# Kernel tuning notes

Hardware: AMD Instinct MI355X
Metric: run time of the kernel (lower is better)

The kernel has to match this reference:

```python
import jax, jax.numpy as jnp
import numpy as np

D = 1024      # in/out token dims
E = 2048      # expanded dim = 2*D
S_ATT = 128   # attention feature dim s
EPS = 1e-5
SQRT_S = np.sqrt(S_ATT).astype(np.float32)


def setup_inputs() -> dict:
    key = jax.random.key(0)
    ks = jax.random.split(key, 8)
    B, S = 4, 2048
    x = jax.random.normal(ks[0], (B, S, D), dtype=jnp.float32)
    pos_enc = jax.random.normal(ks[1], (S, S_ATT), dtype=jnp.float32)
    # uv Linear: xavier_uniform on weight of shape [2e+s, D]
    fan_out = 2 * E + S_ATT
    limit = np.sqrt(6.0 / (D + fan_out)).astype(np.float32)
    uv_w = jax.random.uniform(ks[2], (fan_out, D), dtype=jnp.float32, minval=-limit, maxval=limit)
    # o Linear: default kaiming-uniform-ish; plain uniform works for a reference
    lim_o = np.sqrt(1.0 / E).astype(np.float32)
    o_w = jax.random.uniform(ks[3], (D, E), dtype=jnp.float32, minval=-lim_o, maxval=lim_o)
    gamma = jax.random.uniform(ks[4], (2, S_ATT), dtype=jnp.float32)
    beta = jax.random.uniform(ks[5], (2, S_ATT), dtype=jnp.float32)
    ln_g = jnp.ones((), dtype=jnp.float32)          # ScaleNorm learnable scalar
    res_scale = jnp.ones((D,), dtype=jnp.float32)   # ChannelWiseScale
    return {"x": x, "pos_enc": pos_enc, "uv_w": uv_w, "o_w": o_w,
            "gamma": gamma, "beta": beta, "ln_g": ln_g, "res_scale": res_scale}


def _gau(x, pos_enc, uv_w, o_w, gamma, beta, ln_g, res_scale):
    # ScaleNorm: x / max(||x|| * d^-0.5, eps) * g
    norm = jnp.linalg.norm(x, axis=-1, keepdims=True) * (D ** -0.5)
    xn = x / jnp.maximum(norm, EPS) * ln_g
    uv = jax.nn.silu(jnp.einsum('bsd,fd->bsf', xn, uv_w))  # [B,S,2E+s]
    u, v, base = uv[..., :E], uv[..., E:2 * E], uv[..., 2 * E:]
    # per-head affine: base[...,None,:]*gamma+beta -> q,k
    qk_base = base[..., None, :] * gamma + beta             # [B,S,2,s]
    q = qk_base[..., 0, :] + pos_enc[None, :, :]            # 'add' pos enc
    k = qk_base[..., 1, :] + pos_enc[None, :, :]
    scores = jnp.einsum('bqs,bks->bqk', q, k) / SQRT_S
    kernel = jnp.square(jax.nn.relu(scores))                # squared-ReLU attention
    attn_v = jnp.einsum('bqk,bke->bqe', kernel, v)
    out = jnp.einsum('bqe,de->bqd', u * attn_v, o_w)
    # residual shortcut with channel-wise scale (in == out dims)
    return x * res_scale + out


def reference(x, pos_enc, uv_w, o_w, gamma, beta, ln_g, res_scale):
    return _gau(x, pos_enc, uv_w, o_w, gamma, beta, ln_g, res_scale)
```

## Files before the change

kernel.cpp:

```cpp
#include <hip/hip_runtime.h>

typedef unsigned short u16;
typedef __bf16 bf16x8 __attribute__((ext_vector_type(8)));
typedef float f32x4 __attribute__((ext_vector_type(4)));

#define SEQ   2048
#define DDIM  1024
#define EDIM  2048
#define FDIM  4224
#define SATT  128
#define NBATCH 4

__device__ __forceinline__ u16 f2bf(float f) {
  unsigned u = __float_as_uint(f);
  unsigned r = (u + 0x7fffu + ((u >> 16) & 1u)) >> 16;
  return (u16)r;
}
__device__ __forceinline__ float bf2f(u16 v) {
  return __uint_as_float(((unsigned)v) << 16);
}

__device__ __forceinline__ void gload16(const u16* g, u16* l) {
  auto gp = (const __attribute__((address_space(1))) u16*)(unsigned long long)g;
  auto lp = (__attribute__((address_space(3))) u16*)(unsigned)(unsigned long long)l;
  __builtin_amdgcn_global_load_lds(gp, lp, 16, 0, 0);
}


__global__ void cvt_bf16_kernel(const float* __restrict__ in, u16* __restrict__ out, int n4) {
  int i = blockIdx.x * blockDim.x + threadIdx.x;
  if (i >= n4) return;
  float4 v = reinterpret_cast<const float4*>(in)[i];
  unsigned p0 = (unsigned)f2bf(v.x) | ((unsigned)f2bf(v.y) << 16);
  unsigned p1 = (unsigned)f2bf(v.z) | ((unsigned)f2bf(v.w) << 16);
  uint2 pk; pk.x = p0; pk.y = p1;
  reinterpret_cast<uint2*>(out)[i] = pk;
}

__global__ void rms_kernel(const float* __restrict__ x, const float* __restrict__ ln_g,
                           u16* __restrict__ xn) {
  int row = blockIdx.x;
  int t = threadIdx.x;
  const float4* xr = reinterpret_cast<const float4*>(x + (size_t)row * DDIM);
  float4 v = xr[t];
  float s = v.x * v.x + v.y * v.y + v.z * v.z + v.w * v.w;
#pragma unroll
  for (int off = 32; off > 0; off >>= 1) s += __shfl_down(s, off);
  __shared__ float wsum[4];
  int lane = t & 63, wv = t >> 6;
  if (lane == 0) wsum[wv] = s;
  __syncthreads();
  float tot = wsum[0] + wsum[1] + wsum[2] + wsum[3];
  float rms = sqrtf(tot * (1.0f / (float)DDIM));
  float scale = ln_g[0] / fmaxf(rms, 1e-5f);
  unsigned p0 = (unsigned)f2bf(v.x * scale) | ((unsigned)f2bf(v.y * scale) << 16);
  unsigned p1 = (unsigned)f2bf(v.z * scale) | ((unsigned)f2bf(v.w * scale) << 16);
  uint2 pk; pk.x = p0; pk.y = p1;
  reinterpret_cast<uint2*>(xn + (size_t)row * DDIM)[t] = pk;
}

__global__ void qk_kernel(const u16* __restrict__ uv, const float* __restrict__ pos_enc,
                          const float* __restrict__ gamma, const float* __restrict__ beta,
                          u16* __restrict__ q, u16* __restrict__ k, int ldF) {
  int r = blockIdx.x;
  int t = threadIdx.x;
  int s = r & (SEQ - 1);
  float bval = bf2f(uv[(size_t)r * ldF + 2 * EDIM + t]);
  float pe = pos_enc[(size_t)s * SATT + t];
  float qv = bval * gamma[t] + beta[t] + pe;
  float kv = bval * gamma[SATT + t] + beta[SATT + t] + pe;
  q[(size_t)r * SATT + t] = f2bf(qv);
  k[(size_t)r * SATT + t] = f2bf(kv);
}

__global__ void transpose_v(const u16* __restrict__ uv, u16* __restrict__ vt, int ldF) {
  __shared__ u16 tile[32][33];
  int b = blockIdx.z;
  uv += (size_t)b * SEQ * ldF;
  vt += (size_t)b * EDIM * SEQ;
  int e0 = blockIdx.x * 32, s0 = blockIdx.y * 32;
  int tx = threadIdx.x, ty = threadIdx.y;
#pragma unroll
  for (int j = 0; j < 32; j += 8)
    tile[ty + j][tx] = uv[(size_t)(s0 + ty + j) * ldF + EDIM + e0 + tx];
  __syncthreads();
#pragma unroll
  for (int j = 0; j < 32; j += 8)
    vt[(size_t)(e0 + ty + j) * SEQ + s0 + tx] = tile[tx][ty + j];
}

template <int EPI>
__global__ __launch_bounds__(512, 2) void gemm_bt3(
    const u16* __restrict__ A, const u16* __restrict__ B,
    int N, int K,
    u16* __restrict__ Cbf,
    const u16* __restrict__ U, int ldu,
    size_t sA, size_t sB, size_t sC, size_t sU) {
  __shared__ u16 lds[65536];
  const int tid = threadIdx.x;
  const int w = tid >> 6, l = tid & 63;
  const int wm2 = w >> 2, wn2 = w & 3;
  const int fr = l & 15, kg = l >> 4;

  const int bz = blockIdx.z;
  A += (size_t)bz * sA; B += (size_t)bz * sB; U += (size_t)bz * sU;

  const int nbx = gridDim.x;
  int li = blockIdx.y * nbx + blockIdx.x;
  const int cpx = (nbx * gridDim.y) >> 3;
  li = (li & 7) * cpx + (li >> 3);
  const int bn = li % nbx;
  const int bm = li / nbx;

  const int NT = K >> 6;
  const bool full = (bn * 256 + 256 <= N);

  const int r0 = (w << 3) + (l >> 3);
  const int cswz = (((l & 7) ^ (l >> 3)) & 7) << 3;

  const u16* pA00 = A + (size_t)bm * 256 * K + (size_t)r0 * K + cswz;
  const u16* pA01 = pA00 + (size_t)64 * K;
  const u16* pA10 = pA00 + (size_t)128 * K;
  const u16* pA11 = pA00 + (size_t)192 * K;
  const u16* pB00 = B + (size_t)bn * 256 * K + (size_t)r0 * K + cswz;
  const u16* pB01 = pB00 + (size_t)64 * K;
  const u16* pB10 = pB00 + (size_t)128 * K;
  const u16* pB11 = pB00 + (size_t)192 * K;

  const int X  = (l & 7) << 4;
  const int Y0 = (kg << 4) ^ X;
  const int Y1 = ((kg << 4) | 64) ^ X;
  const char* ldsC = (const char*)lds;
  const char* aR[2][2];
  const char* bR[2][2];
  aR[0][0] = ldsC + wm2 * 8192 + fr * 128 + Y0;
  aR[0][1] = ldsC + wm2 * 8192 + fr * 128 + Y1;
  aR[1][0] = aR[0][0] + 65536;
  aR[1][1] = aR[0][1] + 65536;
  bR[0][0] = ldsC + 32768 + wn2 * 4096 + fr * 128 + Y0;
  bR[0][1] = ldsC + 32768 + wn2 * 4096 + fr * 128 + Y1;
  bR[1][0] = bR[0][0] + 65536;
  bR[1][1] = bR[0][1] + 65536;

  auto stg = [&](int bufw, int p, const u16* g0, const u16* g1, int ofs) {
    u16* d = lds + bufw * 32768 + p * 8192 + w * 512;
    gload16(g0 + ofs, d);
    gload16(g1 + ofs, d + 4096);
  };

  f32x4 acc[8][4];
#pragma unroll
  for (int i = 0; i < 8; i++)
#pragma unroll
    for (int j = 0; j < 4; j++) acc[i][j] = f32x4{0.f, 0.f, 0.f, 0.f};

  stg(0, 0, pA00, pA01, 0); stg(0, 2, pB00, pB01, 0);
  if (full) stg(0, 3, pB10, pB11, 0);
  stg(0, 1, pA10, pA11, 0);
  if (NT > 1) {
    stg(1, 0, pA00, pA01, 64); stg(1, 2, pB00, pB01, 64);
    if (full) stg(1, 3, pB10, pB11, 64);
    stg(1, 1, pA10, pA11, 64);
    if (full) asm volatile("s_waitcnt vmcnt(8)" ::: "memory");
    else      asm volatile("s_waitcnt vmcnt(6)" ::: "memory");
  } else {
    asm volatile("s_waitcnt vmcnt(0)" ::: "memory");
  }
  __builtin_amdgcn_s_barrier();

  bf16x8 aH[4][2], bF[2][2][2];

#define MFMA_Q(QA, QB)                                                        \
  _Pragma("unroll") for (int s = 0; s < 2; s++)                               \
  _Pragma("unroll") for (int i = 0; i < 4; i++)                               \
  _Pragma("unroll") for (int j = 0; j < 2; j++)                               \
    acc[(QA)*4 + i][(QB)*2 + j] = __builtin_amdgcn_mfma_f32_16x16x32_bf16(    \
        aH[i][s], bF[QB][j][s], acc[(QA)*4 + i][(QB)*2 + j], 0, 0, 0);

#define TILE_STEP(BUF, ST, OFS)                                               \
  {                                                                           \
                                  \
    _Pragma("unroll") for (int i = 0; i < 4; i++)                             \
    _Pragma("unroll") for (int s = 0; s < 2; s++)                             \
      aH[i][s] = *(const bf16x8*)(aR[BUF][s] + i * 2048);                     \
    _Pragma("unroll") for (int j = 0; j < 2; j++)                             \
    _Pragma("unroll") for (int s = 0; s < 2; s++)                             \
      bF[0][j][s] = *(const bf16x8*)(bR[BUF][s] + j * 2048);                  \
    asm volatile("s_waitcnt lgkmcnt(8)" ::: "memory");                        \
    __builtin_amdgcn_s_barrier();                                             \
    asm volatile("s_waitcnt lgkmcnt(0)" ::: "memory");                        \
    __builtin_amdgcn_s_setprio(1);                                            \
    MFMA_Q(0, 0)                                                              \
    __builtin_amdgcn_s_setprio(0);                                            \
    __builtin_amdgcn_s_barrier();                                             \
                   \
    if (full) {                                                               \
      _Pragma("unroll") for (int j = 0; j < 2; j++)                           \
      _Pragma("unroll") for (int s = 0; s < 2; s++)                           \
        bF[1][j][s] = *(const bf16x8*)(bR[BUF][s] + 16384 + j * 2048);        \
    }                                                                         \
    if (ST) { stg(BUF, 0, pA00, pA01, OFS); stg(BUF, 2, pB00, pB01, OFS); }   \
    __builtin_amdgcn_s_barrier();                                             \
    asm volatile("s_waitcnt lgkmcnt(0)" ::: "memory");                        \
    __builtin_amdgcn_s_setprio(1);                                            \
    if (full) { MFMA_Q(0, 1) }                                                \
    __builtin_amdgcn_s_setprio(0);                                            \
    __builtin_amdgcn_s_barrier();                                             \
                        \
    _Pragma("unroll") for (int i = 0; i < 4; i++)                             \
    _Pragma("unroll") for (int s = 0; s < 2; s++)                             \
      aH[i][s] = *(const bf16x8*)(aR[BUF][s] + 16384 + i * 2048);             \
    if ((ST) && full) { stg(BUF, 3, pB10, pB11, OFS); }                       \
    __builtin_amdgcn_s_barrier();                                             \
    asm volatile("s_waitcnt lgkmcnt(0)" ::: "memory");                        \
    __builtin_amdgcn_s_setprio(1);                                            \
    MFMA_Q(1, 0)                                                              \
    __builtin_amdgcn_s_setprio(0);                                            \
    __builtin_amdgcn_s_barrier();                                             \
                      \
    if (ST) { stg(BUF, 1, pA10, pA11, OFS); }                                 \
    __builtin_amdgcn_s_setprio(1);                                            \
    if (full) { MFMA_Q(1, 1) }                                                \
    __builtin_amdgcn_s_setprio(0);                                            \
    if (ST) asm volatile("s_waitcnt vmcnt(6)" ::: "memory");                  \
    else    asm volatile("s_waitcnt vmcnt(0)" ::: "memory");                  \
    __builtin_amdgcn_s_barrier();                                             \
  }

  for (int t2 = 0; t2 < NT; t2 += 2) {
    const bool st0 = (t2 + 2 < NT);
    const bool st1 = (t2 + 3 < NT);
    TILE_STEP(0, st0, 128)
    TILE_STEP(1, st1, 192)
    pA00 += 128; pA01 += 128; pA10 += 128; pA11 += 128;
    pB00 += 128; pB01 += 128; pB10 += 128; pB11 += 128;
  }
#undef TILE_STEP
#undef MFMA_Q

  const int rsub = (l >> 4) * 4;
  const int ccol = l & 15;
#pragma unroll
  for (int ai = 0; ai < 8; ai++) {
#pragma unroll
    for (int bj = 0; bj < 4; bj++) {
      if (!full && bj >= 2) continue;
      int n = bn * 256 + (bj >> 1) * 128 + wn2 * 32 + (bj & 1) * 16 + ccol;
#pragma unroll
      for (int tt = 0; tt < 4; tt++) {
        int m = bm * 256 + (ai >> 2) * 128 + wm2 * 64 + (ai & 3) * 16 + rsub + tt;
        float v = acc[ai][bj][tt];
        size_t idx = (size_t)m * N + n;
        if constexpr (EPI == 0) {
          float sv = v / (1.f + __expf(-v));
          Cbf[(size_t)bz * sC + idx] = f2bf(sv);
        } else if constexpr (EPI == 1) {
          float sc = v * 0.08838834764831845f;
          sc = sc > 0.f ? sc * sc : 0.f;
          Cbf[(size_t)bz * sC + idx] = f2bf(sc);
        } else {
          float uvl = bf2f(U[(size_t)m * ldu + n]);
          Cbf[(size_t)bz * sC + idx] = f2bf(v * uvl);
        }
      }
    }
  }
}

template <int EPI>
__global__ __launch_bounds__(512, 2) void gemm_bt2(
    const u16* __restrict__ A, const u16* __restrict__ B,
    int M, int N, int K,
    u16* __restrict__ Cbf, float* __restrict__ Cf,
    const u16* __restrict__ U, int ldu,
    const float* __restrict__ Xres, const float* __restrict__ rscale,
    size_t sA, size_t sB, size_t sC, size_t sU) {
  __shared__ u16 lds[3 * 24576];
  const int tid = threadIdx.x;
  const int w = tid >> 6, l = tid & 63;
  const int wr = w >> 1, wc = w & 1;
  const int fr = l & 15, kg = l >> 4;

  const int bz = blockIdx.z;
  A += (size_t)bz * sA; B += (size_t)bz * sB; U += (size_t)bz * sU;

  const int nbx = gridDim.x;
  int li = blockIdx.y * nbx + blockIdx.x;
  const int cpx = (nbx * gridDim.y) >> 3;
  li = (li & 7) * cpx + (li >> 3);
  const int bn = li % nbx;
  const int bm = li / nbx;

  const int NT = K >> 6;
  const int srow = (w << 3) + (l >> 3);
  const int scol = (((l & 7) ^ (l >> 3)) & 7) << 3;
  const size_t aoff = (size_t)bm * 256 * K;
  const size_t boff = (size_t)bn * 128 * K;
  const char* ldsC = (const char*)lds;

  auto stageAu = [&](int t, int h) {
    int sb = (t % 3) * 24576 + h * 8192;
    const u16* g = A + aoff + (size_t)(h * 128 + srow) * K + t * 64 + scol;
#pragma unroll
    for (int L = 0; L < 2; L++)
      gload16(g + (size_t)(L * 64) * K, &lds[sb + (L * 8 + w) * 512]);
  };
  auto stageBu = [&](int t) {
    int sb = (t % 3) * 24576 + 16384;
    const u16* g = B + boff + (size_t)srow * K + t * 64 + scol;
#pragma unroll
    for (int L = 0; L < 2; L++)
      gload16(g + (size_t)(L * 64) * K, &lds[sb + (L * 8 + w) * 512]);
  };
  auto ldA = [&](int cur, int i, int s) -> bf16x8 {
    int r = ((wr & 1) << 6) + (i << 4) + fr;
    int off = cur * 49152 + ((wr >> 1) << 14) + (r << 7) + (s << 6) + (kg << 4);
    off ^= (r & 7) << 4;
    return *(const bf16x8*)(ldsC + off);
  };
  auto ldB = [&](int cur, int j, int s) -> bf16x8 {
    int r = (wc << 6) + (j << 4) + fr;
    int off = cur * 49152 + 32768 + (r << 7) + (s << 6) + (kg << 4);
    off ^= (r & 7) << 4;
    return *(const bf16x8*)(ldsC + off);
  };

  f32x4 acc[4][4];
#pragma unroll
  for (int i = 0; i < 4; i++)
#pragma unroll
    for (int j = 0; j < 4; j++) acc[i][j] = f32x4{0.f, 0.f, 0.f, 0.f};

  stageAu(0, 0); stageAu(0, 1); stageBu(0);
  if (NT > 1) { stageAu(1, 0); stageAu(1, 1); stageBu(1); }
  asm volatile("s_waitcnt vmcnt(6)" ::: "memory");
  __builtin_amdgcn_s_barrier();

  bf16x8 aF[2][2], bF[2][2][2];
  for (int t = 0; t < NT; ++t) {
    const int cur = t % 3;
    const bool st = (t + 2 < NT);
#pragma unroll
    for (int i = 0; i < 2; i++)
#pragma unroll
      for (int s = 0; s < 2; s++) aF[i][s] = ldA(cur, i, s);
#pragma unroll
    for (int j = 0; j < 2; j++)
#pragma unroll
      for (int s = 0; s < 2; s++) bF[0][j][s] = ldB(cur, j, s);
    if (st) stageAu(t + 2, 0);
    __builtin_amdgcn_s_barrier();
    __builtin_amdgcn_s_setprio(1);
#pragma unroll
    for (int s = 0; s < 2; s++)
#pragma unroll
      for (int i = 0; i < 2; i++)
#pragma unroll
        for (int j = 0; j < 2; j++)
          acc[i][j] = __builtin_amdgcn_mfma_f32_16x16x32_bf16(aF[i][s], bF[0][j][s], acc[i][j], 0, 0, 0);
    __builtin_amdgcn_s_setprio(0);
    __builtin_amdgcn_s_barrier();
#pragma unroll
    for (int j = 0; j < 2; j++)
#pragma unroll
      for (int s = 0; s < 2; s++) bF[1][j][s] = ldB(cur, 2 + j, s);
    if (st) stageAu(t + 2, 1);
    __builtin_amdgcn_s_barrier();
    __builtin_amdgcn_s_setprio(1);
#pragma unroll
    for (int s = 0; s < 2; s++)
#pragma unroll
      for (int i = 0; i < 2; i++)
#pragma unroll
        for (int j = 0; j < 2; j++)
          acc[i][2 + j] = __builtin_amdgcn_mfma_f32_16x16x32_bf16(aF[i][s], bF[1][j][s], acc[i][2 + j], 0, 0, 0);
    __builtin_amdgcn_s_setprio(0);
    __builtin_amdgcn_s_barrier();
#pragma unroll
    for (int i = 0; i < 2; i++)
#pragma unroll
      for (int s = 0; s < 2; s++) aF[i][s] = ldA(cur, 2 + i, s);
    if (st) stageBu(t + 2);
    __builtin_amdgcn_s_barrier();
    __builtin_amdgcn_s_setprio(1);
#pragma unroll
    for (int s = 0; s < 2; s++)
#pragma unroll
      for (int i = 0; i < 2; i++)
#pragma unroll
        for (int j = 0; j < 2; j++)
          acc[2 + i][j] = __builtin_amdgcn_mfma_f32_16x16x32_bf16(aF[i][s], bF[0][j][s], acc[2 + i][j], 0, 0, 0);
    __builtin_amdgcn_s_setprio(0);
    __builtin_amdgcn_s_barrier();
    __builtin_amdgcn_s_setprio(1);
#pragma unroll
    for (int s = 0; s < 2; s++)
#pragma unroll
      for (int i = 0; i < 2; i++)
#pragma unroll
        for (int j = 0; j < 2; j++)
          acc[2 + i][2 + j] = __builtin_amdgcn_mfma_f32_16x16x32_bf16(aF[i][s], bF[1][j][s], acc[2 + i][2 + j], 0, 0, 0);
    __builtin_amdgcn_s_setprio(0);
    if (st) asm volatile("s_waitcnt vmcnt(6)" ::: "memory");
    else    asm volatile("s_waitcnt vmcnt(0)" ::: "memory");
    __builtin_amdgcn_s_barrier();
  }

  const int m0 = bm * 256 + wr * 64;
  const int n0 = bn * 128 + wc * 64;
  const int rsub = (l >> 4) * 4;
  const int ccol = l & 15;
#pragma unroll
  for (int i = 0; i < 4; i++) {
#pragma unroll
    for (int j = 0; j < 4; j++) {
      int n = n0 + j * 16 + ccol;
#pragma unroll
      for (int tt = 0; tt < 4; tt++) {
        int m = m0 + i * 16 + rsub + tt;
        float v = acc[i][j][tt];
        size_t idx = (size_t)m * N + n;
        if constexpr (EPI == 0) {
          float sv = v / (1.f + __expf(-v));
          Cbf[(size_t)bz * sC + idx] = f2bf(sv);
        } else if constexpr (EPI == 1) {
          float sc = v * 0.08838834764831845f;
          sc = sc > 0.f ? sc * sc : 0.f;
          Cbf[(size_t)bz * sC + idx] = f2bf(sc);
        } else if constexpr (EPI == 2) {
          float uvl = bf2f(U[(size_t)m * ldu + n]);
          Cbf[(size_t)bz * sC + idx] = f2bf(v * uvl);
        } else {
          Cf[idx] = Xres[idx] * rscale[n] + v;
        }
      }
    }
  }
}

template <int EPI>
__global__ __launch_bounds__(256) void gemm_bt(
    const u16* __restrict__ A, const u16* __restrict__ B,
    int M, int N, int K,
    u16* __restrict__ Cbf, float* __restrict__ Cf,
    const u16* __restrict__ U, int ldu,
    const float* __restrict__ Xres, const float* __restrict__ rscale,
    size_t sA, size_t sB, size_t sC, size_t sU) {
  __shared__ u16 As[128 * 32];
  __shared__ u16 Bs[128 * 32];
  const int tid = threadIdx.x;
  const int wave = tid >> 6, lane = tid & 63;
  const int wr = wave >> 1, wc = wave & 1;
  const int bz = blockIdx.z;
  A += (size_t)bz * sA; B += (size_t)bz * sB; U += (size_t)bz * sU;
  const int nbx = gridDim.x;
  int li = blockIdx.y * nbx + blockIdx.x;
  const int cpx = (nbx * gridDim.y) >> 3;
  li = (li & 7) * cpx + (li >> 3);
  const int bn = li % nbx;
  const int bm = li / nbx;
  const size_t abase = (size_t)bm * 128 * K;
  const size_t bbase = (size_t)bn * 128 * K;
  const int srow = tid >> 2;
  const int scol = (tid & 3) * 8;
  f32x4 acc[4][4];
#pragma unroll
  for (int i = 0; i < 4; i++)
#pragma unroll
    for (int j = 0; j < 4; j++) acc[i][j] = f32x4{0.f, 0.f, 0.f, 0.f};
  const int fr = lane & 15;
  const int fk = (lane >> 4) * 8;
  for (int k0 = 0; k0 < K; k0 += 32) {
#pragma unroll
    for (int r = 0; r < 2; r++) {
      const u16* gA = A + abase + (size_t)(r * 64 + srow) * K + k0 + scol;
      const u16* gB = B + bbase + (size_t)(r * 64 + srow) * K + k0 + scol;
      gload16(gA, As + r * 2048 + wave * 512);
      gload16(gB, Bs + r * 2048 + wave * 512);
    }
    __syncthreads();
    bf16x8 af[4], bfr[4];
#pragma unroll
    for (int i = 0; i < 4; i++) {
      af[i]  = *reinterpret_cast<const bf16x8*>(&As[(wr * 64 + i * 16 + fr) * 32 + fk]);
      bfr[i] = *reinterpret_cast<const bf16x8*>(&Bs[(wc * 64 + i * 16 + fr) * 32 + fk]);
    }
#pragma unroll
    for (int i = 0; i < 4; i++)
#pragma unroll
      for (int j = 0; j < 4; j++)
        acc[i][j] = __builtin_amdgcn_mfma_f32_16x16x32_bf16(af[i], bfr[j], acc[i][j], 0, 0, 0);
    __syncthreads();
  }
  const int m0 = bm * 128 + wr * 64;
  const int n0 = bn * 128 + wc * 64;
  const int rsub = (lane >> 4) * 4;
  const int ccol = lane & 15;
#pragma unroll
  for (int i = 0; i < 4; i++) {
#pragma unroll
    for (int j = 0; j < 4; j++) {
      int n = n0 + j * 16 + ccol;
#pragma unroll
      for (int t = 0; t < 4; t++) {
        int m = m0 + i * 16 + rsub + t;
        float v = acc[i][j][t];
        size_t idx = (size_t)m * N + n;
        if constexpr (EPI == 0) {
          float sv = v / (1.f + __expf(-v));
          Cbf[(size_t)bz * sC + idx] = f2bf(sv);
        } else if constexpr (EPI == 1) {
          float sc = v * 0.08838834764831845f;
          sc = sc > 0.f ? sc * sc : 0.f;
          Cbf[(size_t)bz * sC + idx] = f2bf(sc);
        } else if constexpr (EPI == 2) {
          float uvl = bf2f(U[(size_t)m * ldu + n]);
          Cbf[(size_t)bz * sC + idx] = f2bf(v * uvl);
        } else {
          Cf[idx] = Xres[idx] * rscale[n] + v;
        }
      }
    }
  }
}


extern "C" void kernel_launch(void* const* d_in, const int* in_sizes, int n_in,
                              void* d_out, int out_size, void* d_ws, size_t ws_size,
                              hipStream_t stream) {
  const float* x        = (const float*)d_in[0];
  const float* pos_enc  = (const float*)d_in[1];
  const float* uv_w     = (const float*)d_in[2];
  const float* o_w      = (const float*)d_in[3];
  const float* gamma    = (const float*)d_in[4];
  const float* beta     = (const float*)d_in[5];
  const float* ln_g     = (const float*)d_in[6];
  const float* res_scale= (const float*)d_in[7];
  float* out = (float*)d_out;

  auto al = [](size_t b) { return (b + 255) & ~(size_t)255; };
  const size_t SZ_UVW  = (size_t)FDIM * DDIM * 2;
  const size_t SZ_OW   = (size_t)DDIM * EDIM * 2;
  const size_t SZ_Z    = (size_t)NBATCH * SEQ * EDIM * 2;
  const size_t SZ_XN   = (size_t)NBATCH * SEQ * DDIM * 2;
  const size_t SZ_UV   = (size_t)NBATCH * SEQ * FDIM * 2;
  const size_t SZ_QK   = (size_t)NBATCH * SEQ * SATT * 2;
  const size_t SZ_VT1  = (size_t)EDIM * SEQ * 2;
  const size_t SZ_P1   = (size_t)SEQ * SEQ * 2;
  const size_t need_full =
      al(SZ_UVW) + al(SZ_OW) + al(SZ_Z) + al(SZ_XN) + al(SZ_UV) + 2 * al(SZ_QK) +
      (size_t)NBATCH * (al(SZ_VT1) + al(SZ_P1));
  const bool FULL = ws_size >= need_full;

  char* p = (char*)d_ws;
  auto alloc = [&](size_t bytes) {
    char* r = p;
    p += (bytes + 255) & ~(size_t)255;
    return r;
  };

  if (FULL) {
    u16* uvw_bf = (u16*)alloc(SZ_UVW);
    u16* ow_bf  = (u16*)alloc(SZ_OW);
    u16* z      = (u16*)alloc(SZ_Z);
    u16* vt     = (u16*)alloc((size_t)NBATCH * al(SZ_VT1));
    u16* pmat   = (u16*)alloc((size_t)NBATCH * al(SZ_P1));
    u16* xn     = (u16*)alloc(SZ_XN);
    u16* uv     = (u16*)alloc(SZ_UV);
    u16* qb     = (u16*)alloc(SZ_QK);
    u16* kb     = (u16*)alloc(SZ_QK);
    const size_t sVT = al(SZ_VT1) >> 1;
    const size_t sP  = al(SZ_P1) >> 1;
    const int rows = NBATCH * SEQ;

    cvt_bf16_kernel<<<(FDIM * DDIM / 4 + 255) / 256, 256, 0, stream>>>(
        uv_w, uvw_bf, FDIM * DDIM / 4);
    cvt_bf16_kernel<<<(DDIM * EDIM / 4 + 255) / 256, 256, 0, stream>>>(
        o_w, ow_bf, DDIM * EDIM / 4);

    rms_kernel<<<rows, 256, 0, stream>>>(x, ln_g, xn);
    gemm_bt3<0><<<dim3(17, rows / 256), 512, 0, stream>>>(
        xn, uvw_bf, FDIM, DDIM, uv, nullptr, 0, 0, 0, 0, 0);
    qk_kernel<<<rows, SATT, 0, stream>>>(uv, pos_enc, gamma, beta, qb, kb, FDIM);
    transpose_v<<<dim3(EDIM / 32, SEQ / 32, NBATCH), dim3(32, 8), 0, stream>>>(uv, vt, FDIM);
    gemm_bt3<1><<<dim3(SEQ / 256, SEQ / 256, NBATCH), 512, 0, stream>>>(
        qb, kb, SEQ, SATT, pmat, nullptr, 0,
        (size_t)SEQ * SATT, (size_t)SEQ * SATT, sP, 0);
    gemm_bt3<2><<<dim3(EDIM / 256, SEQ / 256, NBATCH), 512, 0, stream>>>(
        pmat, vt, EDIM, SEQ, z, uv, FDIM,
        sP, sVT, (size_t)SEQ * EDIM, (size_t)SEQ * FDIM);
    gemm_bt2<3><<<dim3(DDIM / 128, rows / 256), 512, 0, stream>>>(
        z, ow_bf, rows, DDIM, EDIM, nullptr, out, nullptr, 0,
        x, res_scale, 0, 0, 0, 0);
    return;
  }

  u16* uvw_bf = (u16*)alloc(SZ_UVW);
  u16* ow_bf  = (u16*)alloc(SZ_OW);
  u16* z      = (u16*)alloc(SZ_Z);
  u16* vt     = (u16*)alloc(SZ_VT1);
  u16* pmat   = (u16*)alloc(SZ_P1);
  size_t fixed = (size_t)(p - (char*)d_ws);
  const size_t perbc = (size_t)SEQ * DDIM * 2 + (size_t)SEQ * FDIM * 2 +
                       2 * (size_t)SEQ * SATT * 2 + 4 * 256;
  int BC = (ws_size >= fixed + 4 * perbc) ? 4 : 1;
  u16* xn = (u16*)alloc((size_t)BC * SEQ * DDIM * 2);
  u16* uv = (u16*)alloc((size_t)BC * SEQ * FDIM * 2);
  u16* qb = (u16*)alloc((size_t)BC * SEQ * SATT * 2);
  u16* kb = (u16*)alloc((size_t)BC * SEQ * SATT * 2);

  cvt_bf16_kernel<<<(FDIM * DDIM / 4 + 255) / 256, 256, 0, stream>>>(
      uv_w, uvw_bf, FDIM * DDIM / 4);
  cvt_bf16_kernel<<<(DDIM * EDIM / 4 + 255) / 256, 256, 0, stream>>>(
      o_w, ow_bf, DDIM * EDIM / 4);

  for (int b0 = 0; b0 < NBATCH; b0 += BC) {
    int rows = BC * SEQ;
    rms_kernel<<<rows, 256, 0, stream>>>(x + (size_t)b0 * SEQ * DDIM, ln_g, xn);
    gemm_bt<0><<<dim3(FDIM / 128, rows / 128), 256, 0, stream>>>(
        xn, uvw_bf, rows, FDIM, DDIM, uv, nullptr, nullptr, 0, nullptr, nullptr,
        0, 0, 0, 0);
    qk_kernel<<<rows, SATT, 0, stream>>>(uv, pos_enc, gamma, beta, qb, kb, FDIM);
    for (int bb = 0; bb < BC; bb++) {
      int b = b0 + bb;
      const u16* uvb = uv + (size_t)bb * SEQ * FDIM;
      transpose_v<<<dim3(EDIM / 32, SEQ / 32, 1), dim3(32, 8), 0, stream>>>(uvb, vt, FDIM);
      gemm_bt<1><<<dim3(SEQ / 128, SEQ / 128), 256, 0, stream>>>(
          qb + (size_t)bb * SEQ * SATT, kb + (size_t)bb * SEQ * SATT,
          SEQ, SEQ, SATT, pmat, nullptr, nullptr, 0, nullptr, nullptr,
          0, 0, 0, 0);
      gemm_bt<2><<<dim3(EDIM / 128, SEQ / 128), 256, 0, stream>>>(
          pmat, vt, SEQ, EDIM, SEQ, z + (size_t)b * SEQ * EDIM, nullptr,
          uvb, FDIM, nullptr, nullptr, 0, 0, 0, 0);
    }
  }
  gemm_bt<3><<<dim3(DDIM / 128, (NBATCH * SEQ) / 128), 256, 0, stream>>>(
      z, ow_bf, NBATCH * SEQ, DDIM, EDIM, nullptr, out, nullptr, 0,
      x, res_scale, 0, 0, 0, 0);
}
```

Measured before the change: 280.4 us.

## Replace staged ping-pong GEMM schedule with simple one-ahead double buffering

Replaces the GEMM main loop's interleaved schedule with a plain double-buffered loop. The old loop used four barrier-separated phases, a two-tile global prefetch depth, partial vmcnt waits and s_setprio. The new loop issues all global-to-LDS loads for the next tile at the start of each step, then reads the current buffer and runs all MFMA quadrants. It finishes each step with a full vmcnt(0) wait, a barrier and a sched_barrier. This removes many barriers and lets the compiler schedule LDS reads, at the cost of only one tile of prefetch lookahead and a full memory drain every step.

After: 273.3 us. 2.5% less time.

```diff
diff --git a/kernel.cpp b/kernel.cpp
--- a/kernel.cpp
+++ b/kernel.cpp
@@ -131,16 +131,10 @@
   const int Y0 = (kg << 4) ^ X;
   const int Y1 = ((kg << 4) | 64) ^ X;
   const char* ldsC = (const char*)lds;
-  const char* aR[2][2];
-  const char* bR[2][2];
-  aR[0][0] = ldsC + wm2 * 8192 + fr * 128 + Y0;
-  aR[0][1] = ldsC + wm2 * 8192 + fr * 128 + Y1;
-  aR[1][0] = aR[0][0] + 65536;
-  aR[1][1] = aR[0][1] + 65536;
-  bR[0][0] = ldsC + 32768 + wn2 * 4096 + fr * 128 + Y0;
-  bR[0][1] = ldsC + 32768 + wn2 * 4096 + fr * 128 + Y1;
-  bR[1][0] = bR[0][0] + 65536;
-  bR[1][1] = bR[0][1] + 65536;
+  const char* aR0 = ldsC + wm2 * 8192 + fr * 128 + Y0;
+  const char* aR1 = ldsC + wm2 * 8192 + fr * 128 + Y1;
+  const char* bR0 = ldsC + 32768 + wn2 * 4096 + fr * 128 + Y0;
+  const char* bR1 = ldsC + 32768 + wn2 * 4096 + fr * 128 + Y1;
 
   auto stg = [&](int bufw, int p, const u16* g0, const u16* g1, int ofs) {
     u16* d = lds + bufw * 32768 + p * 8192 + w * 512;
@@ -157,16 +151,9 @@
   stg(0, 0, pA00, pA01, 0); stg(0, 2, pB00, pB01, 0);
   if (full) stg(0, 3, pB10, pB11, 0);
   stg(0, 1, pA10, pA11, 0);
-  if (NT > 1) {
-    stg(1, 0, pA00, pA01, 64); stg(1, 2, pB00, pB01, 64);
-    if (full) stg(1, 3, pB10, pB11, 64);
-    stg(1, 1, pA10, pA11, 64);
-    if (full) asm volatile("s_waitcnt vmcnt(8)" ::: "memory");
-    else      asm volatile("s_waitcnt vmcnt(6)" ::: "memory");
-  } else {
-    asm volatile("s_waitcnt vmcnt(0)" ::: "memory");
-  }
+  asm volatile("s_waitcnt vmcnt(0)" ::: "memory");
   __builtin_amdgcn_s_barrier();
+  __builtin_amdgcn_sched_barrier(0);
 
   bf16x8 aH[4][2], bF[2][2][2];
 
@@ -179,59 +166,47 @@
 
 #define TILE_STEP(BUF, ST, OFS)                                               \
   {                                                                           \
-                                  \
-    _Pragma("unroll") for (int i = 0; i < 4; i++)                             \
-    _Pragma("unroll") for (int s = 0; s < 2; s++)                             \
-      aH[i][s] = *(const bf16x8*)(aR[BUF][s] + i * 2048);                     \
-    _Pragma("unroll") for (int j = 0; j < 2; j++)                             \
-    _Pragma("unroll") for (int s = 0; s < 2; s++)                             \
-      bF[0][j][s] = *(const bf16x8*)(bR[BUF][s] + j * 2048);                  \
-    asm volatile("s_waitcnt lgkmcnt(8)" ::: "memory");                        \
+                     \
+    if (ST) {                                                                 \
+      stg((BUF) ^ 1, 0, pA00, pA01, OFS);                                     \
+      stg((BUF) ^ 1, 2, pB00, pB01, OFS);                                     \
+      if (full) stg((BUF) ^ 1, 3, pB10, pB11, OFS);                           \
+      stg((BUF) ^ 1, 1, pA10, pA11, OFS);                                     \
+    }                                                                         \
+       \
+    _Pragma("unroll") for (int i = 0; i < 4; i++) {                           \
+      aH[i][0] = *(const bf16x8*)(aR0 + (BUF) * 65536 + i * 2048);            \
+      aH[i][1] = *(const bf16x8*)(aR1 + (BUF) * 65536 + i * 2048);            \
+    }                                                                         \
+    _Pragma("unroll") for (int j = 0; j < 2; j++) {                           \
+      bF[0][j][0] = *(const bf16x8*)(bR0 + (BUF) * 65536 + j * 2048);         \
+      bF[0][j][1] = *(const bf16x8*)(bR1 + (BUF) * 65536 + j * 2048);         \
+    }                                                                         \
+    MFMA_Q(0, 0)                                                              \
+    if (full) {                                                               \
+      _Pragma("unroll") for (int j = 0; j < 2; j++) {                         \
+        bF[1][j][0] = *(const bf16x8*)(bR0 + (BUF) * 65536 + 16384 + j * 2048);\
+        bF[1][j][1] = *(const bf16x8*)(bR1 + (BUF) * 65536 + 16384 + j * 2048);\
+      }                                                                       \
+      MFMA_Q(0, 1)                                                            \
+    }                                                                         \
+    _Pragma("unroll") for (int i = 0; i < 4; i++) {                           \
+      aH[i][0] = *(const bf16x8*)(aR0 + (BUF) * 65536 + 16384 + i * 2048);    \
+      aH[i][1] = *(const bf16x8*)(aR1 + (BUF) * 65536 + 16384 + i * 2048);    \
+    }                                                                         \
+    MFMA_Q(1, 0)                                                              \
+    if (full) { MFMA_Q(1, 1) }                                                \
+           \
+    asm volatile("s_waitcnt vmcnt(0)" ::: "memory");                          \
     __builtin_amdgcn_s_barrier();                                             \
-    asm volatile("s_waitcnt lgkmcnt(0)" ::: "memory");                        \
-    __builtin_amdgcn_s_setprio(1);                                            \
-    MFMA_Q(0, 0)                                                              \
-    __builtin_amdgcn_s_setprio(0);                                            \
-    __builtin_amdgcn_s_barrier();                                             \
-                   \
-    if (full) {                                                               \
-      _Pragma("unroll") for (int j = 0; j < 2; j++)                           \
-      _Pragma("unroll") for (int s = 0; s < 2; s++)                           \
-        bF[1][j][s] = *(const bf16x8*)(bR[BUF][s] + 16384 + j * 2048);        \
-    }                                                                         \
-    if (ST) { stg(BUF, 0, pA00, pA01, OFS); stg(BUF, 2, pB00, pB01, OFS); }   \
-    __builtin_amdgcn_s_barrier();                                             \
-    asm volatile("s_waitcnt lgkmcnt(0)" ::: "memory");                        \
-    __builtin_amdgcn_s_setprio(1);                                            \
-    if (full) { MFMA_Q(0, 1) }                                                \
-    __builtin_amdgcn_s_setprio(0);                                            \
-    __builtin_amdgcn_s_barrier();                                             \
-                        \
-    _Pragma("unroll") for (int i = 0; i < 4; i++)                             \
-    _Pragma("unroll") for (int s = 0; s < 2; s++)                             \
-      aH[i][s] = *(const bf16x8*)(aR[BUF][s] + 16384 + i * 2048);             \
-    if ((ST) && full) { stg(BUF, 3, pB10, pB11, OFS); }                       \
-    __builtin_amdgcn_s_barrier();                                             \
-    asm volatile("s_waitcnt lgkmcnt(0)" ::: "memory");                        \
-    __builtin_amdgcn_s_setprio(1);                                            \
-    MFMA_Q(1, 0)                                                              \
-    __builtin_amdgcn_s_setprio(0);                                            \
-    __builtin_amdgcn_s_barrier();                                             \
-                      \
-    if (ST) { stg(BUF, 1, pA10, pA11, OFS); }                                 \
-    __builtin_amdgcn_s_setprio(1);                                            \
-    if (full) { MFMA_Q(1, 1) }                                                \
-    __builtin_amdgcn_s_setprio(0);                                            \
-    if (ST) asm volatile("s_waitcnt vmcnt(6)" ::: "memory");                  \
-    else    asm volatile("s_waitcnt vmcnt(0)" ::: "memory");                  \
-    __builtin_amdgcn_s_barrier();                                             \
+    __builtin_amdgcn_sched_barrier(0);                                        \
   }
 
   for (int t2 = 0; t2 < NT; t2 += 2) {
-    const bool st0 = (t2 + 2 < NT);
-    const bool st1 = (t2 + 3 < NT);
-    TILE_STEP(0, st0, 128)
-    TILE_STEP(1, st1, 192)
+    const bool st0 = (t2 + 1 < NT);
+    const bool st1 = (t2 + 2 < NT);
+    TILE_STEP(0, st0, 64)
+    TILE_STEP(1, st1, 128)
     pA00 += 128; pA01 += 128; pA10 += 128; pA11 += 128;
     pB00 += 128; pB01 += 128; pB10 += 128; pB11 += 128;
   }
```
